# Kernel tuning notes

Measured on AMD Instinct MI355X. Metric: run time of the kernel, lower is better.

## Reference

```python
import jax, jax.numpy as jnp
import numpy as np

FEAT_STRIDE = 16
NEG_THR, POS_THR = 0.3, 0.7        # cfg.TRAIN.RPN_NEGATIVE_OVERLAP / RPN_POSITIVE_OVERLAP
RPN_BATCHSIZE, NUM_FG = 256, 128   # RPN_BATCHSIZE, FG_FRACTION=0.5
A_PER_LOC = 9


def generate_anchors(base_size=16, ratios=(0.5, 1.0, 2.0), scales=(8, 16, 32)):
    w = h = float(base_size)
    xc = yc = 0.5 * (base_size - 1)
    size = w * h
    ws = np.round(np.sqrt(size / np.array(ratios)))
    hs = np.round(ws * np.array(ratios))
    out = []
    for wi, hi in zip(ws, hs):
        for s in scales:
            W, H = wi * s, hi * s
            out.append([xc - 0.5 * (W - 1), yc - 0.5 * (H - 1),
                        xc + 0.5 * (W - 1), yc + 0.5 * (H - 1)])
    return np.array(out, dtype=np.float32)  # [9, 4]


def _forward(rpn_cls_score, gt_boxes, im_info):
    B, _, H, W = rpn_cls_score.shape
    A = A_PER_LOC
    base = jnp.asarray(generate_anchors())
    sx, sy = jnp.meshgrid(jnp.arange(W) * FEAT_STRIDE, jnp.arange(H) * FEAT_STRIDE)  # 'xy', [H,W]
    shifts = jnp.stack([sx.ravel(), sy.ravel(), sx.ravel(), sy.ravel()], 1).astype(jnp.float32)  # [K,4]
    anchors = (base[None, :, :] + shifts[:, None, :]).reshape(-1, 4)  # [N=K*A, 4], (h,w,a)-major
    N = anchors.shape[0]

    img_h, img_w = im_info[0, 0], im_info[0, 1]
    inside = ((anchors[:, 0] >= 0) & (anchors[:, 1] >= 0) &
              (anchors[:, 2] < img_w) & (anchors[:, 3] < img_h))  # [N]

    # ---- IoU overlaps (torch +1 pixel convention) ----
    gt = gt_boxes[..., :4]  # [B,Kg,4]
    aw = anchors[:, 2] - anchors[:, 0] + 1.0
    ah = anchors[:, 3] - anchors[:, 1] + 1.0
    a_area = aw * ah                                   # [N]
    g_area = (gt[..., 2] - gt[..., 0] + 1.0) * (gt[..., 3] - gt[..., 1] + 1.0)  # [B,Kg]
    ix = jnp.maximum(0.0, jnp.minimum(anchors[None, :, None, 2], gt[:, None, :, 2])
                     - jnp.maximum(anchors[None, :, None, 0], gt[:, None, :, 0]) + 1.0)
    iy = jnp.maximum(0.0, jnp.minimum(anchors[None, :, None, 3], gt[:, None, :, 3])
                     - jnp.maximum(anchors[None, :, None, 1], gt[:, None, :, 1]) + 1.0)
    inter = ix * iy
    ovr = inter / (a_area[None, :, None] + g_area[:, None, :] - inter)  # [B,N,Kg]

    max_ovr = ovr.max(2)
    arg = ovr.argmax(2)                                 # [B,N]
    ovr_in = jnp.where(inside[None, :, None], ovr, 0.0)  # only in-image anchors compete for gt-max
    gt_max = ovr_in.max(1)                              # [B,Kg]
    gt_max = jnp.where(gt_max == 0.0, 1e-5, gt_max)
    is_best = (ovr_in == gt_max[:, None, :]).any(2)     # [B,N]

    # ---- label assignment (RPN_CLOBBER_POSITIVES = False) ----
    lbl = jnp.full((B, N), -1.0, jnp.float32)
    lbl = jnp.where(inside[None] & (max_ovr < NEG_THR), 0.0, lbl)
    lbl = jnp.where(inside[None] & is_best, 1.0, lbl)
    lbl = jnp.where(inside[None] & (max_ovr >= POS_THR), 1.0, lbl)

    # ---- random fg/bg subsampling (deterministic jax PRNG replaces np.random.permutation) ----
    def _subsample(lbl_b, key):
        kf, kb = jax.random.split(key)
        def disable(l, mask, limit, k):
            prio = jnp.where(mask, jax.random.uniform(k, l.shape), -1.0)
            order = jnp.argsort(-prio)
            rank = jnp.zeros(l.shape[0], jnp.int32).at[order].set(jnp.arange(l.shape[0], dtype=jnp.int32))
            return jnp.where(mask & (rank >= limit), -1.0, l)
        lbl_b = disable(lbl_b, lbl_b == 1.0, NUM_FG, kf)
        num_bg = RPN_BATCHSIZE - jnp.sum(lbl_b == 1.0)
        return disable(lbl_b, lbl_b == 0.0, num_bg, kb)

    lbl = jax.vmap(_subsample)(lbl, jax.random.split(jax.random.key(42), B))

    assigned = jnp.take_along_axis(gt, arg[..., None], axis=1)  # [B,N,4]
    acx = anchors[:, 0] + 0.5 * (aw - 1.0)
    acy = anchors[:, 1] + 0.5 * (ah - 1.0)
    g_w = assigned[..., 2] - assigned[..., 0] + 1.0
    g_h = assigned[..., 3] - assigned[..., 1] + 1.0
    gcx = assigned[..., 0] + 0.5 * (g_w - 1.0)
    gcy = assigned[..., 1] + 0.5 * (g_h - 1.0)
    targets = jnp.stack([(gcx - acx[None]) / aw[None], (gcy - acy[None]) / ah[None],
                         jnp.log(g_w / aw[None]), jnp.log(g_h / ah[None])], -1)  # [B,N,4]

    in_w = jnp.where(lbl == 1.0, 1.0, 0.0)             # RPN_BBOX_INSIDE_WEIGHTS = 1
    num_examples = jnp.sum(lbl >= 0.0, axis=1).astype(jnp.float32)  # RPN_POSITIVE_WEIGHT = -1
    uw = 1.0 / num_examples                             # uniform pos/neg weight, per batch
    out_w = jnp.where((lbl == 1.0) | (lbl == 0.0), uw[:, None], 0.0)

    # ---- _unmap with fill=0 for out-of-image anchors ----
    lbl = jnp.where(inside[None], lbl, 0.0)
    targets = jnp.where(inside[None, :, None], targets, 0.0)
    in_w = jnp.where(inside[None], in_w, 0.0)
    out_w = jnp.where(inside[None], out_w, 0.0)

    labels_out = lbl.reshape(B, H, W, A).transpose(0, 3, 1, 2).reshape(B, 1, A * H, W)
    targets_out = targets.reshape(B, H, W, 4 * A).transpose(0, 3, 1, 2)
    in_w_out = jnp.broadcast_to(in_w[..., None], (B, N, 4)).reshape(B, H, W, 4 * A).transpose(0, 3, 1, 2)
    out_w_out = jnp.broadcast_to(out_w[..., None], (B, N, 4)).reshape(B, H, W, 4 * A).transpose(0, 3, 1, 2)
    return labels_out, targets_out, in_w_out, out_w_out


def setup_inputs() -> dict:
    key = jax.random.key(0)
    B, A, H, W, Kg = 16, 9, 64, 64, 50
    k1, k2, k3, k4, k5 = jax.random.split(key, 5)
    rpn_cls_score = jax.random.normal(k1, (B, 2 * A, H, W), jnp.float32)
    # valid GT boxes inside a 1024x1024 image, class label in column 4
    x1 = jax.random.uniform(k2, (B, Kg)) * 800.0
    y1 = jax.random.uniform(k3, (B, Kg)) * 800.0
    w = 20.0 + jax.random.uniform(k4, (B, Kg)) * 200.0
    h = 20.0 + jax.random.uniform(k5, (B, Kg)) * 200.0
    cls = jnp.ones((B, Kg), jnp.float32)
    gt_boxes = jnp.stack([x1, y1, x1 + w, y1 + h, cls], -1)
    im_info = jnp.full((B, 2), 1024.0, jnp.float32)
    return {"rpn_cls_score": rpn_cls_score, "gt_boxes": gt_boxes, "im_info": im_info, "num_boxes": Kg}


def reference(rpn_cls_score, gt_boxes, im_info, num_boxes):
    return _forward(rpn_cls_score, gt_boxes, im_info)
```

## Files before the change

### kernel.cpp

```cpp
#include <hip/hip_runtime.h>
#include <stdint.h>


#define B_   16
#define A_   9
#define H_   64
#define W_   64
#define HW_  (H_*W_)
#define N_   (HW_*A_)
#define KG_  50
#define S0_  (B_*A_*HW_)
#define S1_  (B_*4*A_*HW_)
#define NGTB_ (B_*KG_)
#define CAP_  20480
#define NHIST_ (B_*2*256 + B_*2)

typedef unsigned long long ull;

__constant__ float c_base[A_][4] = {
  { -84.f,  -40.f,  99.f,  55.f},
  {-176.f,  -88.f, 191.f, 103.f},
  {-360.f, -184.f, 375.f, 199.f},
  { -56.f,  -56.f,  71.f,  71.f},
  {-120.f, -120.f, 135.f, 135.f},
  {-248.f, -248.f, 263.f, 263.f},
  { -36.f,  -80.f,  51.f,  95.f},
  { -80.f, -168.f,  95.f, 183.f},
  {-168.f, -344.f, 183.f, 359.f},
};

__device__ __forceinline__ void tf2x32(uint32_t k0, uint32_t k1,
                                       uint32_t x0, uint32_t x1,
                                       uint32_t& o0, uint32_t& o1) {
  const uint32_t ks2 = k0 ^ k1 ^ 0x1BD11BDAu;
  uint32_t ks[3] = {k0, k1, ks2};
  x0 += ks[0]; x1 += ks[1];
  const int R[2][4] = {{13,15,26,6},{17,29,16,24}};
  #pragma unroll
  for (int i = 0; i < 5; i++) {
    #pragma unroll
    for (int j = 0; j < 4; j++) {
      x0 += x1;
      int r = R[i & 1][j];
      x1 = (x1 << r) | (x1 >> (32 - r));
      x1 ^= x0;
    }
    x0 += ks[(i + 1) % 3];
    x1 += ks[(i + 2) % 3] + (uint32_t)(i + 1);
  }
  o0 = x0; o1 = x1;
}

__device__ __attribute__((noinline))
float box_area_f(float x1, float y1, float x2, float y2) {
#pragma clang fp contract(off)
  return (x2 - x1 + 1.f) * (y2 - y1 + 1.f);
}

__device__ __attribute__((noinline))
float iou_core(float ax1, float ay1, float ax2, float ay2, float aarea,
               float gx1, float gy1, float gx2, float gy2, float garea) {
#pragma clang fp contract(off)
  float ix = fmaxf(fminf(ax2, gx2) - fmaxf(ax1, gx1) + 1.f, 0.f);
  float iy = fmaxf(fminf(ay2, gy2) - fmaxf(ay1, gy1) + 1.f, 0.f);
  float inter = ix * iy;
  return inter / (aarea + garea - inter);
}

__global__ __launch_bounds__(256) void k_gtmax(const float* __restrict__ gtb,
                                               const float* __restrict__ iminfo,
                                               float* __restrict__ gt_max,
                                               uint32_t* __restrict__ keys,
                                               int* __restrict__ cnt_hist) {
  const int b = blockIdx.x / KG_;
  const int g = blockIdx.x % KG_;
  const int tid = threadIdx.x;
  if (blockIdx.x == 0 && tid < B_) {
    uint32_t k0, k1, kf0, kf1, kb0, kb1;
    tf2x32(0u, 42u, 0u, (uint32_t)tid, k0, k1);
    tf2x32(k0, k1, 0u, 0u, kf0, kf1);
    tf2x32(k0, k1, 0u, 1u, kb0, kb1);
    keys[tid * 4 + 0] = kf0;
    keys[tid * 4 + 1] = kf1;
    keys[tid * 4 + 2] = kb0;
    keys[tid * 4 + 3] = kb1;
  }
  if (blockIdx.x < 32) {
    const int per = (NHIST_ + 31) / 32;
    const int base = blockIdx.x * per;
    const int lim = min(base + per, NHIST_);
    for (int i = base + tid; i < lim; i += 256) cnt_hist[i] = 0;
  }
  const float* gp = gtb + (b * KG_ + g) * 5;
  const float gx1 = gp[0], gy1 = gp[1], gx2 = gp[2], gy2 = gp[3];
  const float garea = box_area_f(gx1, gy1, gx2, gy2);
  const float imh = iminfo[0], imw = iminfo[1];
  float best = 0.f;
  for (int a = 0; a < A_; a++) {
    const float bx1 = c_base[a][0], by1 = c_base[a][1];
    const float bx2 = c_base[a][2], by2 = c_base[a][3];
    const float aarea = box_area_f(bx1, by1, bx2, by2);
    int xlo = max(0, (int)ceilf(-bx1 / 16.f));
    int xhi = min(W_ - 1, (int)ceilf((imw - bx2) / 16.f) - 1);
    int ylo = max(0, (int)ceilf(-by1 / 16.f));
    int yhi = min(H_ - 1, (int)ceilf((imh - by2) / 16.f) - 1);
    xlo = max(xlo, (int)floorf((gx1 - 1.f - bx2) / 16.f));
    xhi = min(xhi, (int)ceilf((gx2 + 1.f - bx1) / 16.f));
    ylo = max(ylo, (int)floorf((gy1 - 1.f - by2) / 16.f));
    yhi = min(yhi, (int)ceilf((gy2 + 1.f - by1) / 16.f));
    const int nx = xhi - xlo + 1, ny = yhi - ylo + 1;
    if (nx <= 0 || ny <= 0) continue;
    const int lw = (nx <= 1) ? 0 : (32 - __clz(nx - 1));
    const int tot = ny << lw;
    const int mask = (1 << lw) - 1;
    for (int t = tid; t < tot; t += 256) {
      const int xi = t & mask;
      if (xi >= nx) continue;
      const int x = xlo + xi;
      const int y = ylo + (t >> lw);
      const float sx = 16.f * (float)x, sy = 16.f * (float)y;
      best = fmaxf(best, iou_core(bx1 + sx, by1 + sy, bx2 + sx, by2 + sy,
                                  aarea, gx1, gy1, gx2, gy2, garea));
    }
  }
  best = fmaxf(best, __shfl_xor(best, 32));
  best = fmaxf(best, __shfl_xor(best, 16));
  best = fmaxf(best, __shfl_xor(best, 8));
  best = fmaxf(best, __shfl_xor(best, 4));
  best = fmaxf(best, __shfl_xor(best, 2));
  best = fmaxf(best, __shfl_xor(best, 1));
  __shared__ float sw[4];
  if ((tid & 63) == 0) sw[tid >> 6] = best;
  __syncthreads();
  if (tid == 0)
    gt_max[b * KG_ + g] = fmaxf(fmaxf(sw[0], sw[1]), fmaxf(sw[2], sw[3]));
}

__global__ __launch_bounds__(256) void k_fuse(const float* __restrict__ gtb,
                                              const float* __restrict__ iminfo,
                                              const float* __restrict__ gt_max,
                                              const uint32_t* __restrict__ keys,
                                              int* __restrict__ packed,
                                              ull* __restrict__ cand,
                                              int* __restrict__ cnt,
                                              int* __restrict__ hist) {
  __shared__ float sgx1[KG_], sgy1[KG_], sgx2[KG_], sgy2[KG_], sga[KG_], sgm[KG_];
  __shared__ int s_xlo[A_], s_ylo[A_], s_nx[A_], s_pre[A_ + 1];
  __shared__ uint32_t s_k[4];
  __shared__ int s_num[2], s_base[2];
  const int b = blockIdx.y;
  const int tid = threadIdx.x;
  if (tid < KG_) {
    const float* g = gtb + (b * KG_ + tid) * 5;
    float x1 = g[0], y1 = g[1], x2 = g[2], y2 = g[3];
    sgx1[tid] = x1; sgy1[tid] = y1; sgx2[tid] = x2; sgy2[tid] = y2;
    sga[tid] = box_area_f(x1, y1, x2, y2);
    float gm = gt_max[b * KG_ + tid];
    sgm[tid] = (gm == 0.f) ? 1e-5f : gm;
  }
  if (tid < 4) s_k[tid] = keys[b * 4 + tid];
  if (tid < A_) {
    const float imh = iminfo[0], imw = iminfo[1];
    const float bx1 = c_base[tid][0], by1 = c_base[tid][1];
    const float bx2 = c_base[tid][2], by2 = c_base[tid][3];
    int xlo = max(0, (int)ceilf(-bx1 / 16.f));
    int xhi = min(W_ - 1, (int)ceilf((imw - bx2) / 16.f) - 1);
    int ylo = max(0, (int)ceilf(-by1 / 16.f));
    int yhi = min(H_ - 1, (int)ceilf((imh - by2) / 16.f) - 1);
    int nx = max(0, xhi - xlo + 1), ny = max(0, yhi - ylo + 1);
    s_xlo[tid] = xlo; s_ylo[tid] = ylo; s_nx[tid] = nx;
    s_pre[tid + 1] = nx * ny;
  }
  __syncthreads();
  if (tid == 0) {
    s_pre[0] = 0;
    for (int a = 0; a < A_; a++) s_pre[a + 1] += s_pre[a];
  }
  __syncthreads();
  const int C = s_pre[A_];
  const int stride = gridDim.x * 256;

  for (int t0 = blockIdx.x * 256; t0 < C; t0 += stride) {
    if (tid < 2) s_num[tid] = 0;
    __syncthreads();
    const int t = t0 + tid;
    bool act = false;
    int p = 0, lpos = 0, n = 0;
    uint32_t m = 0;
    if (t < C) {
      int a = 0;
      while (t >= s_pre[a + 1]) a++;
      const int idx = t - s_pre[a];
      const int nx = s_nx[a];
      const int y = s_ylo[a] + idx / nx;
      const int x = s_xlo[a] + (idx - (idx / nx) * nx);
      n = (y * W_ + x) * A_ + a;
      const int n2 = a * HW_ + y * W_ + x;
      const float sx = 16.f * (float)x, sy = 16.f * (float)y;
      const float ax1 = c_base[a][0] + sx, ay1 = c_base[a][1] + sy;
      const float ax2 = c_base[a][2] + sx, ay2 = c_base[a][3] + sy;
      const float aarea = box_area_f(c_base[a][0], c_base[a][1],
                                     c_base[a][2], c_base[a][3]);
      float mo = -1.f;
      int bidx = 0;
      bool best = false;
      for (int k = 0; k < KG_; k++) {
        float ovr = iou_core(ax1, ay1, ax2, ay2, aarea,
                             sgx1[k], sgy1[k], sgx2[k], sgy2[k], sga[k]);
        if (ovr > mo) { mo = ovr; bidx = k; }
        best = best || (ovr == sgm[k]);
      }
      int lab = -1;
      if (mo < 0.3f) lab = 0;
      if (best || mo >= 0.7f) lab = 1;
      packed[(size_t)b * N_ + n2] = (bidx << 2) | (lab + 1);
      if (lab >= 0) {
        act = true;
        p = (lab == 1) ? 0 : 1;
        uint32_t y0, y1;
        tf2x32(s_k[2 * p], s_k[2 * p + 1], 0u, (uint32_t)n, y0, y1);
        m = (y0 ^ y1) >> 9;
        lpos = atomicAdd(&s_num[p], 1);
      }
    }
    __syncthreads();
    if (tid < 2 && s_num[tid] > 0)
      s_base[tid] = atomicAdd(&cnt[b * 2 + tid], s_num[tid]);
    __syncthreads();
    if (act) {
      cand[(size_t)(b * 2 + p) * CAP_ + s_base[p] + lpos] =
          ((ull)m << 16) | (ull)(65535 - n);
      atomicAdd(&hist[(b * 2 + p) * 256 + (int)(m >> 15)], 1);
    }
    __syncthreads();
  }
}

__global__ __launch_bounds__(256) void k_select(const ull* __restrict__ cand,
                                                const int* __restrict__ cnt,
                                                const int* __restrict__ hist,
                                                ull* __restrict__ Kstar,
                                                float* __restrict__ uw) {
  const int b = blockIdx.x >> 1, p = blockIdx.x & 1;
  const int tid = threadIdx.x;
  __shared__ ull s_keys[2048];
  __shared__ int s_bin, s_r, s_n;
  const int cf = cnt[b * 2 + 0], cb = cnt[b * 2 + 1];
  const int limit = (p == 0) ? 128 : 256 - min(cf, 128);
  const int c = (p == 0) ? cf : cb;
  if (p == 1 && tid == 0) {
    int kf = min(cf, 128);
    int kb = min(cb, 256 - kf);
    uw[b] = 1.f / (float)(kf + kb);
  }
  if (c <= limit) {
    if (tid == 0) Kstar[b * 2 + p] = 0ull;
    return;
  }
  if (tid == 0) {
    const int* Hh = hist + (b * 2 + p) * 256;
    int acc = 0, bin = 255, r = 0;
    for (; bin >= 0; bin--) {
      int hv = Hh[bin];
      if (acc + hv >= limit) { r = limit - acc; break; }
      acc += hv;
    }
    s_bin = bin; s_r = r; s_n = 0;
  }
  __syncthreads();
  const uint32_t bin0 = (uint32_t)s_bin;
  const int r0 = s_r;
  const ull* C = cand + (size_t)(b * 2 + p) * CAP_;
  for (int i = tid; i < c; i += 256) {
    ull k = C[i];
    if ((uint32_t)(k >> 31) == bin0) {
      int pos = atomicAdd(&s_n, 1);
      if (pos < 2048) s_keys[pos] = k;
    }
  }
  __syncthreads();
  const int s = min(s_n, 2048);
  for (int j = tid; j < s; j += 256) {
    ull kj = s_keys[j];
    int rank = 0;
    for (int q = 0; q < s; q++) rank += (s_keys[q] > kj) ? 1 : 0;
    if (rank == r0 - 1) Kstar[b * 2 + p] = kj;
  }
}

__global__ __launch_bounds__(256) void k_out(const float* __restrict__ gtb,
                                             const float* __restrict__ iminfo,
                                             const int* __restrict__ packed,
                                             const ull* __restrict__ Kstar,
                                             const float* __restrict__ uw,
                                             const uint32_t* __restrict__ keys,
                                             float* __restrict__ out) {
  const int gid = blockIdx.x * 256 + threadIdx.x;
  const int e = gid * 4;
  const int w0 = e & 63;
  const int h = (e >> 6) & 63;
  const int a = (e >> 12) % A_;
  const int b = e / (A_ * HW_);

  const float imh = iminfo[0], imw = iminfo[1];
  const float ay1 = c_base[a][1] + 16.f * (float)h;
  const float ay2 = c_base[a][3] + 16.f * (float)h;
  const bool insY = (ay1 >= 0.f) && (ay2 < imh);

  const int4 pk4 = *(const int4*)(packed + e);
  const int pk[4] = {pk4.x, pk4.y, pk4.z, pk4.w};
  const float uwb = uw[b];
  const ull KF_ = Kstar[b * 2 + 0];
  const ull KB_ = Kstar[b * 2 + 1];
  const uint32_t kf0 = keys[b * 4 + 0], kf1 = keys[b * 4 + 1];
  const uint32_t kb0 = keys[b * 4 + 2], kb1 = keys[b * 4 + 3];

  float4 lab4, tx4, ty4, tw4, th4, inw4, oww4;
  float* labp = (float*)&lab4;
  float* txp = (float*)&tx4; float* typ = (float*)&ty4;
  float* twp = (float*)&tw4; float* thp = (float*)&th4;
  float* inwp = (float*)&inw4; float* owwp = (float*)&oww4;

  #pragma unroll
  for (int j = 0; j < 4; j++) {
    const int w = w0 + j;
    const float ax1 = c_base[a][0] + 16.f * (float)w;
    const float ax2 = c_base[a][2] + 16.f * (float)w;
    const bool ins = insY && (ax1 >= 0.f) && (ax2 < imw);
    int lab = (pk[j] & 3) - 1;
    const int g = pk[j] >> 2;
    float tx = 0.f, ty = 0.f, tw = 0.f, th = 0.f;
    if (ins) {
      if (lab >= 0) {
        const int n = (h * W_ + w) * A_ + a;
        const int p = (lab == 1) ? 0 : 1;
        uint32_t y0, y1;
        tf2x32(p ? kb0 : kf0, p ? kb1 : kf1, 0u, (uint32_t)n, y0, y1);
        ull key = ((ull)((y0 ^ y1) >> 9) << 16) | (ull)(65535 - n);
        if (key < (p ? KB_ : KF_)) lab = -1;
      }
      const float* gp = gtb + ((size_t)b * KG_ + g) * 5;
      float aw = ax2 - ax1 + 1.f, ah = ay2 - ay1 + 1.f;
      float acx = ax1 + 0.5f * (aw - 1.f), acy = ay1 + 0.5f * (ah - 1.f);
      float gw = gp[2] - gp[0] + 1.f, gh = gp[3] - gp[1] + 1.f;
      float gcx = gp[0] + 0.5f * (gw - 1.f), gcy = gp[1] + 0.5f * (gh - 1.f);
      tx = (gcx - acx) / aw;
      ty = (gcy - acy) / ah;
      tw = logf(gw / aw);
      th = logf(gh / ah);
    }
    labp[j] = ins ? (float)lab : 0.f;
    txp[j] = tx; typ[j] = ty; twp[j] = tw; thp[j] = th;
    inwp[j] = (ins && lab == 1) ? 1.f : 0.f;
    owwp[j] = (ins && lab >= 0) ? uwb : 0.f;
  }

  *(float4*)(out + e) = lab4;
  float* o1 = out + S0_;
  const size_t toff = (size_t)b * (4 * A_ * HW_) + (4 * a) * HW_ + h * W_ + w0;
  *(float4*)(o1 + toff)           = tx4;
  *(float4*)(o1 + toff + HW_)     = ty4;
  *(float4*)(o1 + toff + 2 * HW_) = tw4;
  *(float4*)(o1 + toff + 3 * HW_) = th4;
  float* o2 = out + S0_ + S1_;
  *(float4*)(o2 + toff)           = inw4;
  *(float4*)(o2 + toff + HW_)     = inw4;
  *(float4*)(o2 + toff + 2 * HW_) = inw4;
  *(float4*)(o2 + toff + 3 * HW_) = inw4;
  float* o3 = out + S0_ + 2 * (size_t)S1_;
  *(float4*)(o3 + toff)           = oww4;
  *(float4*)(o3 + toff + HW_)     = oww4;
  *(float4*)(o3 + toff + 2 * HW_) = oww4;
  *(float4*)(o3 + toff + 3 * HW_) = oww4;
}

extern "C" void kernel_launch(void* const* d_in, const int* in_sizes, int n_in,
                              void* d_out, int out_size, void* d_ws, size_t ws_size,
                              hipStream_t stream) {
  const float* gtb = (const float*)d_in[1];
  const float* iminfo = (const float*)d_in[2];
  float* out = (float*)d_out;

  int* packed = (int*)d_ws;
  float* gt_max = (float*)(packed + (size_t)B_ * N_);
  float* uw = gt_max + B_ * KG_;
  uint32_t* keys = (uint32_t*)(uw + B_);
  int* cnt = (int*)(keys + B_ * 4);
  int* hist = cnt + B_ * 2;
  ull* Kstar = (ull*)(hist + B_ * 2 * 256);
  ull* cand = Kstar + B_ * 2;

  k_gtmax<<<NGTB_, 256, 0, stream>>>(gtb, iminfo, gt_max, keys, cnt);
  k_fuse<<<dim3(73, B_), 256, 0, stream>>>(gtb, iminfo, gt_max, keys,
                                           packed, cand, cnt, hist);
  k_select<<<B_ * 2, 256, 0, stream>>>(cand, cnt, hist, Kstar, uw);
  k_out<<<S0_ / 4 / 256, 256, 0, stream>>>(gtb, iminfo, packed, Kstar, uw,
                                           keys, out);
}
```

Measured before the change: 137.1 us.

## Merge four kernel launches into one cooperative kernel with grid syncs

Replaces the gt-max, fuse, select and output kernels with a single cooperative kernel of 576 blocks. The stages are separated by grid.sync(), each stage uses grid-stride loops over its virtual blocks, and shared memory is shared between stages through a union. The aim is to remove three kernel launch gaps and the drain between kernels. In exchange, a grid-wide barrier is needed between stages, the final stage is limited to exactly GRID_*256*4 elements, and every stage runs with a fixed grid size that may not suit it.

```diff
diff --git a/kernel.cpp b/kernel.cpp
--- a/kernel.cpp
+++ b/kernel.cpp
@@ -1,5 +1,8 @@
 #include <hip/hip_runtime.h>
+#include <hip/hip_cooperative_groups.h>
 #include <stdint.h>
+
+namespace cg = cooperative_groups;
 
 
 #define B_   16
@@ -12,6 +15,8 @@
 #define S0_  (B_*A_*HW_)
 #define S1_  (B_*4*A_*HW_)
 #define NGTB_ (B_*KG_)
+#define NFB_  (B_*73)
+#define GRID_ 576
 #define CAP_  20480
 #define NHIST_ (B_*2*256 + B_*2)
 
@@ -67,15 +72,38 @@
   return inter / (aarea + garea - inter);
 }
 
-__global__ __launch_bounds__(256) void k_gtmax(const float* __restrict__ gtb,
-                                               const float* __restrict__ iminfo,
-                                               float* __restrict__ gt_max,
-                                               uint32_t* __restrict__ keys,
-                                               int* __restrict__ cnt_hist) {
-  const int b = blockIdx.x / KG_;
-  const int g = blockIdx.x % KG_;
+__global__ __launch_bounds__(256) void k_mega(const float* __restrict__ gtb,
+                                              const float* __restrict__ iminfo,
+                                              float* __restrict__ out,
+                                              int* __restrict__ packed,
+                                              float* __restrict__ gt_max,
+                                              float* __restrict__ uw,
+                                              uint32_t* __restrict__ keys,
+                                              int* __restrict__ cnt,
+                                              int* __restrict__ hist,
+                                              ull* __restrict__ Kstar,
+                                              ull* __restrict__ cand) {
+  cg::grid_group grid = cg::this_grid();
   const int tid = threadIdx.x;
-  if (blockIdx.x == 0 && tid < B_) {
+  const int bid = blockIdx.x;
+
+  __shared__ union {
+    struct {
+      float sgx1[KG_], sgy1[KG_], sgx2[KG_], sgy2[KG_], sga[KG_], sgm[KG_];
+      int xlo[A_], ylo[A_], nx[A_], pre[A_ + 1];
+      uint32_t k[4];
+      int num[2], base[2];
+    } f;
+    struct {
+      ull keys2[2048];
+      int bin, r, n;
+    } s;
+    float sw[4];
+  } sh;
+
+  const float imh = iminfo[0], imw = iminfo[1];
+
+  if (bid == 0 && tid < B_) {
     uint32_t k0, k1, kf0, kf1, kb0, kb1;
     tf2x32(0u, 42u, 0u, (uint32_t)tid, k0, k1);
     tf2x32(k0, k1, 0u, 0u, kf0, kf1);
@@ -85,115 +113,106 @@
     keys[tid * 4 + 2] = kb0;
     keys[tid * 4 + 3] = kb1;
   }
-  if (blockIdx.x < 32) {
+  if (bid < 32) {
     const int per = (NHIST_ + 31) / 32;
-    const int base = blockIdx.x * per;
+    const int base = bid * per;
     const int lim = min(base + per, NHIST_);
-    for (int i = base + tid; i < lim; i += 256) cnt_hist[i] = 0;
-  }
-  const float* gp = gtb + (b * KG_ + g) * 5;
-  const float gx1 = gp[0], gy1 = gp[1], gx2 = gp[2], gy2 = gp[3];
-  const float garea = box_area_f(gx1, gy1, gx2, gy2);
-  const float imh = iminfo[0], imw = iminfo[1];
-  float best = 0.f;
-  for (int a = 0; a < A_; a++) {
-    const float bx1 = c_base[a][0], by1 = c_base[a][1];
-    const float bx2 = c_base[a][2], by2 = c_base[a][3];
-    const float aarea = box_area_f(bx1, by1, bx2, by2);
-    int xlo = max(0, (int)ceilf(-bx1 / 16.f));
-    int xhi = min(W_ - 1, (int)ceilf((imw - bx2) / 16.f) - 1);
-    int ylo = max(0, (int)ceilf(-by1 / 16.f));
-    int yhi = min(H_ - 1, (int)ceilf((imh - by2) / 16.f) - 1);
-    xlo = max(xlo, (int)floorf((gx1 - 1.f - bx2) / 16.f));
-    xhi = min(xhi, (int)ceilf((gx2 + 1.f - bx1) / 16.f));
-    ylo = max(ylo, (int)floorf((gy1 - 1.f - by2) / 16.f));
-    yhi = min(yhi, (int)ceilf((gy2 + 1.f - by1) / 16.f));
-    const int nx = xhi - xlo + 1, ny = yhi - ylo + 1;
-    if (nx <= 0 || ny <= 0) continue;
-    const int lw = (nx <= 1) ? 0 : (32 - __clz(nx - 1));
-    const int tot = ny << lw;
-    const int mask = (1 << lw) - 1;
-    for (int t = tid; t < tot; t += 256) {
-      const int xi = t & mask;
-      if (xi >= nx) continue;
-      const int x = xlo + xi;
-      const int y = ylo + (t >> lw);
-      const float sx = 16.f * (float)x, sy = 16.f * (float)y;
-      best = fmaxf(best, iou_core(bx1 + sx, by1 + sy, bx2 + sx, by2 + sy,
-                                  aarea, gx1, gy1, gx2, gy2, garea));
-    }
-  }
-  best = fmaxf(best, __shfl_xor(best, 32));
-  best = fmaxf(best, __shfl_xor(best, 16));
-  best = fmaxf(best, __shfl_xor(best, 8));
-  best = fmaxf(best, __shfl_xor(best, 4));
-  best = fmaxf(best, __shfl_xor(best, 2));
-  best = fmaxf(best, __shfl_xor(best, 1));
-  __shared__ float sw[4];
-  if ((tid & 63) == 0) sw[tid >> 6] = best;
-  __syncthreads();
-  if (tid == 0)
-    gt_max[b * KG_ + g] = fmaxf(fmaxf(sw[0], sw[1]), fmaxf(sw[2], sw[3]));
-}
-
-__global__ __launch_bounds__(256) void k_fuse(const float* __restrict__ gtb,
-                                              const float* __restrict__ iminfo,
-                                              const float* __restrict__ gt_max,
-                                              const uint32_t* __restrict__ keys,
-                                              int* __restrict__ packed,
-                                              ull* __restrict__ cand,
-                                              int* __restrict__ cnt,
-                                              int* __restrict__ hist) {
-  __shared__ float sgx1[KG_], sgy1[KG_], sgx2[KG_], sgy2[KG_], sga[KG_], sgm[KG_];
-  __shared__ int s_xlo[A_], s_ylo[A_], s_nx[A_], s_pre[A_ + 1];
-  __shared__ uint32_t s_k[4];
-  __shared__ int s_num[2], s_base[2];
-  const int b = blockIdx.y;
-  const int tid = threadIdx.x;
-  if (tid < KG_) {
-    const float* g = gtb + (b * KG_ + tid) * 5;
-    float x1 = g[0], y1 = g[1], x2 = g[2], y2 = g[3];
-    sgx1[tid] = x1; sgy1[tid] = y1; sgx2[tid] = x2; sgy2[tid] = y2;
-    sga[tid] = box_area_f(x1, y1, x2, y2);
-    float gm = gt_max[b * KG_ + tid];
-    sgm[tid] = (gm == 0.f) ? 1e-5f : gm;
-  }
-  if (tid < 4) s_k[tid] = keys[b * 4 + tid];
-  if (tid < A_) {
-    const float imh = iminfo[0], imw = iminfo[1];
-    const float bx1 = c_base[tid][0], by1 = c_base[tid][1];
-    const float bx2 = c_base[tid][2], by2 = c_base[tid][3];
-    int xlo = max(0, (int)ceilf(-bx1 / 16.f));
-    int xhi = min(W_ - 1, (int)ceilf((imw - bx2) / 16.f) - 1);
-    int ylo = max(0, (int)ceilf(-by1 / 16.f));
-    int yhi = min(H_ - 1, (int)ceilf((imh - by2) / 16.f) - 1);
-    int nx = max(0, xhi - xlo + 1), ny = max(0, yhi - ylo + 1);
-    s_xlo[tid] = xlo; s_ylo[tid] = ylo; s_nx[tid] = nx;
-    s_pre[tid + 1] = nx * ny;
-  }
-  __syncthreads();
-  if (tid == 0) {
-    s_pre[0] = 0;
-    for (int a = 0; a < A_; a++) s_pre[a + 1] += s_pre[a];
-  }
-  __syncthreads();
-  const int C = s_pre[A_];
-  const int stride = gridDim.x * 256;
-
-  for (int t0 = blockIdx.x * 256; t0 < C; t0 += stride) {
-    if (tid < 2) s_num[tid] = 0;
-    __syncthreads();
-    const int t = t0 + tid;
+    for (int i = base + tid; i < lim; i += 256) cnt[i] = 0;
+  }
+  for (int vb = bid; vb < NGTB_; vb += GRID_) {
+    const int b = vb / KG_;
+    const int g = vb % KG_;
+    const float* gp = gtb + (b * KG_ + g) * 5;
+    const float gx1 = gp[0], gy1 = gp[1], gx2 = gp[2], gy2 = gp[3];
+    const float garea = box_area_f(gx1, gy1, gx2, gy2);
+    float best = 0.f;
+    for (int a = 0; a < A_; a++) {
+      const float bx1 = c_base[a][0], by1 = c_base[a][1];
+      const float bx2 = c_base[a][2], by2 = c_base[a][3];
+      const float aarea = box_area_f(bx1, by1, bx2, by2);
+      int xlo = max(0, (int)ceilf(-bx1 / 16.f));
+      int xhi = min(W_ - 1, (int)ceilf((imw - bx2) / 16.f) - 1);
+      int ylo = max(0, (int)ceilf(-by1 / 16.f));
+      int yhi = min(H_ - 1, (int)ceilf((imh - by2) / 16.f) - 1);
+      xlo = max(xlo, (int)floorf((gx1 - 1.f - bx2) / 16.f));
+      xhi = min(xhi, (int)ceilf((gx2 + 1.f - bx1) / 16.f));
+      ylo = max(ylo, (int)floorf((gy1 - 1.f - by2) / 16.f));
+      yhi = min(yhi, (int)ceilf((gy2 + 1.f - by1) / 16.f));
+      const int nx = xhi - xlo + 1, ny = yhi - ylo + 1;
+      if (nx <= 0 || ny <= 0) continue;
+      const int lw = (nx <= 1) ? 0 : (32 - __clz(nx - 1));
+      const int tot = ny << lw;
+      const int mask = (1 << lw) - 1;
+      for (int t = tid; t < tot; t += 256) {
+        const int xi = t & mask;
+        if (xi >= nx) continue;
+        const int x = xlo + xi;
+        const int y = ylo + (t >> lw);
+        const float sx = 16.f * (float)x, sy = 16.f * (float)y;
+        best = fmaxf(best, iou_core(bx1 + sx, by1 + sy, bx2 + sx, by2 + sy,
+                                    aarea, gx1, gy1, gx2, gy2, garea));
+      }
+    }
+    best = fmaxf(best, __shfl_xor(best, 32));
+    best = fmaxf(best, __shfl_xor(best, 16));
+    best = fmaxf(best, __shfl_xor(best, 8));
+    best = fmaxf(best, __shfl_xor(best, 4));
+    best = fmaxf(best, __shfl_xor(best, 2));
+    best = fmaxf(best, __shfl_xor(best, 1));
+    if ((tid & 63) == 0) sh.sw[tid >> 6] = best;
+    __syncthreads();
+    if (tid == 0)
+      gt_max[b * KG_ + g] = fmaxf(fmaxf(sh.sw[0], sh.sw[1]),
+                                  fmaxf(sh.sw[2], sh.sw[3]));
+    __syncthreads();
+  }
+
+  grid.sync();
+
+  for (int vb = bid; vb < NFB_; vb += GRID_) {
+    const int b = vb / 73;
+    const int chunk = vb % 73;
+    __syncthreads();
+    if (tid < KG_) {
+      const float* g = gtb + (b * KG_ + tid) * 5;
+      float x1 = g[0], y1 = g[1], x2 = g[2], y2 = g[3];
+      sh.f.sgx1[tid] = x1; sh.f.sgy1[tid] = y1;
+      sh.f.sgx2[tid] = x2; sh.f.sgy2[tid] = y2;
+      sh.f.sga[tid] = box_area_f(x1, y1, x2, y2);
+      float gm = gt_max[b * KG_ + tid];
+      sh.f.sgm[tid] = (gm == 0.f) ? 1e-5f : gm;
+    }
+    if (tid < 4) sh.f.k[tid] = keys[b * 4 + tid];
+    if (tid < 2) sh.f.num[tid] = 0;
+    if (tid < A_) {
+      const float bx1 = c_base[tid][0], by1 = c_base[tid][1];
+      const float bx2 = c_base[tid][2], by2 = c_base[tid][3];
+      int xlo = max(0, (int)ceilf(-bx1 / 16.f));
+      int xhi = min(W_ - 1, (int)ceilf((imw - bx2) / 16.f) - 1);
+      int ylo = max(0, (int)ceilf(-by1 / 16.f));
+      int yhi = min(H_ - 1, (int)ceilf((imh - by2) / 16.f) - 1);
+      int nx = max(0, xhi - xlo + 1), ny = max(0, yhi - ylo + 1);
+      sh.f.xlo[tid] = xlo; sh.f.ylo[tid] = ylo; sh.f.nx[tid] = nx;
+      sh.f.pre[tid + 1] = nx * ny;
+    }
+    __syncthreads();
+    if (tid == 0) {
+      sh.f.pre[0] = 0;
+      for (int a = 0; a < A_; a++) sh.f.pre[a + 1] += sh.f.pre[a];
+    }
+    __syncthreads();
+    const int C = sh.f.pre[A_];
+    const int t = chunk * 256 + tid;
     bool act = false;
     int p = 0, lpos = 0, n = 0;
     uint32_t m = 0;
     if (t < C) {
       int a = 0;
-      while (t >= s_pre[a + 1]) a++;
-      const int idx = t - s_pre[a];
-      const int nx = s_nx[a];
-      const int y = s_ylo[a] + idx / nx;
-      const int x = s_xlo[a] + (idx - (idx / nx) * nx);
+      while (t >= sh.f.pre[a + 1]) a++;
+      const int idx = t - sh.f.pre[a];
+      const int nx = sh.f.nx[a];
+      const int y = sh.f.ylo[a] + idx / nx;
+      const int x = sh.f.xlo[a] + (idx - (idx / nx) * nx);
       n = (y * W_ + x) * A_ + a;
       const int n2 = a * HW_ + y * W_ + x;
       const float sx = 16.f * (float)x, sy = 16.f * (float)y;
@@ -206,9 +225,10 @@
       bool best = false;
       for (int k = 0; k < KG_; k++) {
         float ovr = iou_core(ax1, ay1, ax2, ay2, aarea,
-                             sgx1[k], sgy1[k], sgx2[k], sgy2[k], sga[k]);
+                             sh.f.sgx1[k], sh.f.sgy1[k],
+                             sh.f.sgx2[k], sh.f.sgy2[k], sh.f.sga[k]);
         if (ovr > mo) { mo = ovr; bidx = k; }
-        best = best || (ovr == sgm[k]);
+        best = best || (ovr == sh.f.sgm[k]);
       }
       int lab = -1;
       if (mo < 0.3f) lab = 0;
@@ -218,160 +238,149 @@
         act = true;
         p = (lab == 1) ? 0 : 1;
         uint32_t y0, y1;
-        tf2x32(s_k[2 * p], s_k[2 * p + 1], 0u, (uint32_t)n, y0, y1);
+        tf2x32(sh.f.k[2 * p], sh.f.k[2 * p + 1], 0u, (uint32_t)n, y0, y1);
         m = (y0 ^ y1) >> 9;
-        lpos = atomicAdd(&s_num[p], 1);
-      }
-    }
-    __syncthreads();
-    if (tid < 2 && s_num[tid] > 0)
-      s_base[tid] = atomicAdd(&cnt[b * 2 + tid], s_num[tid]);
+        lpos = atomicAdd(&sh.f.num[p], 1);
+      }
+    }
+    __syncthreads();
+    if (tid < 2 && sh.f.num[tid] > 0)
+      sh.f.base[tid] = atomicAdd(&cnt[b * 2 + tid], sh.f.num[tid]);
     __syncthreads();
     if (act) {
-      cand[(size_t)(b * 2 + p) * CAP_ + s_base[p] + lpos] =
+      cand[(size_t)(b * 2 + p) * CAP_ + sh.f.base[p] + lpos] =
           ((ull)m << 16) | (ull)(65535 - n);
       atomicAdd(&hist[(b * 2 + p) * 256 + (int)(m >> 15)], 1);
     }
-    __syncthreads();
-  }
-}
-
-__global__ __launch_bounds__(256) void k_select(const ull* __restrict__ cand,
-                                                const int* __restrict__ cnt,
-                                                const int* __restrict__ hist,
-                                                ull* __restrict__ Kstar,
-                                                float* __restrict__ uw) {
-  const int b = blockIdx.x >> 1, p = blockIdx.x & 1;
-  const int tid = threadIdx.x;
-  __shared__ ull s_keys[2048];
-  __shared__ int s_bin, s_r, s_n;
-  const int cf = cnt[b * 2 + 0], cb = cnt[b * 2 + 1];
-  const int limit = (p == 0) ? 128 : 256 - min(cf, 128);
-  const int c = (p == 0) ? cf : cb;
-  if (p == 1 && tid == 0) {
-    int kf = min(cf, 128);
-    int kb = min(cb, 256 - kf);
-    uw[b] = 1.f / (float)(kf + kb);
-  }
-  if (c <= limit) {
-    if (tid == 0) Kstar[b * 2 + p] = 0ull;
-    return;
-  }
-  if (tid == 0) {
-    const int* Hh = hist + (b * 2 + p) * 256;
-    int acc = 0, bin = 255, r = 0;
-    for (; bin >= 0; bin--) {
-      int hv = Hh[bin];
-      if (acc + hv >= limit) { r = limit - acc; break; }
-      acc += hv;
-    }
-    s_bin = bin; s_r = r; s_n = 0;
-  }
-  __syncthreads();
-  const uint32_t bin0 = (uint32_t)s_bin;
-  const int r0 = s_r;
-  const ull* C = cand + (size_t)(b * 2 + p) * CAP_;
-  for (int i = tid; i < c; i += 256) {
-    ull k = C[i];
-    if ((uint32_t)(k >> 31) == bin0) {
-      int pos = atomicAdd(&s_n, 1);
-      if (pos < 2048) s_keys[pos] = k;
-    }
-  }
-  __syncthreads();
-  const int s = min(s_n, 2048);
-  for (int j = tid; j < s; j += 256) {
-    ull kj = s_keys[j];
-    int rank = 0;
-    for (int q = 0; q < s; q++) rank += (s_keys[q] > kj) ? 1 : 0;
-    if (rank == r0 - 1) Kstar[b * 2 + p] = kj;
-  }
-}
-
-__global__ __launch_bounds__(256) void k_out(const float* __restrict__ gtb,
-                                             const float* __restrict__ iminfo,
-                                             const int* __restrict__ packed,
-                                             const ull* __restrict__ Kstar,
-                                             const float* __restrict__ uw,
-                                             const uint32_t* __restrict__ keys,
-                                             float* __restrict__ out) {
-  const int gid = blockIdx.x * 256 + threadIdx.x;
-  const int e = gid * 4;
-  const int w0 = e & 63;
-  const int h = (e >> 6) & 63;
-  const int a = (e >> 12) % A_;
-  const int b = e / (A_ * HW_);
-
-  const float imh = iminfo[0], imw = iminfo[1];
-  const float ay1 = c_base[a][1] + 16.f * (float)h;
-  const float ay2 = c_base[a][3] + 16.f * (float)h;
-  const bool insY = (ay1 >= 0.f) && (ay2 < imh);
-
-  const int4 pk4 = *(const int4*)(packed + e);
-  const int pk[4] = {pk4.x, pk4.y, pk4.z, pk4.w};
-  const float uwb = uw[b];
-  const ull KF_ = Kstar[b * 2 + 0];
-  const ull KB_ = Kstar[b * 2 + 1];
-  const uint32_t kf0 = keys[b * 4 + 0], kf1 = keys[b * 4 + 1];
-  const uint32_t kb0 = keys[b * 4 + 2], kb1 = keys[b * 4 + 3];
-
-  float4 lab4, tx4, ty4, tw4, th4, inw4, oww4;
-  float* labp = (float*)&lab4;
-  float* txp = (float*)&tx4; float* typ = (float*)&ty4;
-  float* twp = (float*)&tw4; float* thp = (float*)&th4;
-  float* inwp = (float*)&inw4; float* owwp = (float*)&oww4;
-
-  #pragma unroll
-  for (int j = 0; j < 4; j++) {
-    const int w = w0 + j;
-    const float ax1 = c_base[a][0] + 16.f * (float)w;
-    const float ax2 = c_base[a][2] + 16.f * (float)w;
-    const bool ins = insY && (ax1 >= 0.f) && (ax2 < imw);
-    int lab = (pk[j] & 3) - 1;
-    const int g = pk[j] >> 2;
-    float tx = 0.f, ty = 0.f, tw = 0.f, th = 0.f;
-    if (ins) {
-      if (lab >= 0) {
-        const int n = (h * W_ + w) * A_ + a;
-        const int p = (lab == 1) ? 0 : 1;
-        uint32_t y0, y1;
-        tf2x32(p ? kb0 : kf0, p ? kb1 : kf1, 0u, (uint32_t)n, y0, y1);
-        ull key = ((ull)((y0 ^ y1) >> 9) << 16) | (ull)(65535 - n);
-        if (key < (p ? KB_ : KF_)) lab = -1;
-      }
-      const float* gp = gtb + ((size_t)b * KG_ + g) * 5;
-      float aw = ax2 - ax1 + 1.f, ah = ay2 - ay1 + 1.f;
-      float acx = ax1 + 0.5f * (aw - 1.f), acy = ay1 + 0.5f * (ah - 1.f);
-      float gw = gp[2] - gp[0] + 1.f, gh = gp[3] - gp[1] + 1.f;
-      float gcx = gp[0] + 0.5f * (gw - 1.f), gcy = gp[1] + 0.5f * (gh - 1.f);
-      tx = (gcx - acx) / aw;
-      ty = (gcy - acy) / ah;
-      tw = logf(gw / aw);
-      th = logf(gh / ah);
-    }
-    labp[j] = ins ? (float)lab : 0.f;
-    txp[j] = tx; typ[j] = ty; twp[j] = tw; thp[j] = th;
-    inwp[j] = (ins && lab == 1) ? 1.f : 0.f;
-    owwp[j] = (ins && lab >= 0) ? uwb : 0.f;
-  }
-
-  *(float4*)(out + e) = lab4;
-  float* o1 = out + S0_;
-  const size_t toff = (size_t)b * (4 * A_ * HW_) + (4 * a) * HW_ + h * W_ + w0;
-  *(float4*)(o1 + toff)           = tx4;
-  *(float4*)(o1 + toff + HW_)     = ty4;
-  *(float4*)(o1 + toff + 2 * HW_) = tw4;
-  *(float4*)(o1 + toff + 3 * HW_) = th4;
-  float* o2 = out + S0_ + S1_;
-  *(float4*)(o2 + toff)           = inw4;
-  *(float4*)(o2 + toff + HW_)     = inw4;
-  *(float4*)(o2 + toff + 2 * HW_) = inw4;
-  *(float4*)(o2 + toff + 3 * HW_) = inw4;
-  float* o3 = out + S0_ + 2 * (size_t)S1_;
-  *(float4*)(o3 + toff)           = oww4;
-  *(float4*)(o3 + toff + HW_)     = oww4;
-  *(float4*)(o3 + toff + 2 * HW_) = oww4;
-  *(float4*)(o3 + toff + 3 * HW_) = oww4;
+  }
+
+  grid.sync();
+
+  if (bid < B_ * 2) {
+    const int b = bid >> 1, p = bid & 1;
+    const int cf = cnt[b * 2 + 0], cb = cnt[b * 2 + 1];
+    const int limit = (p == 0) ? 128 : 256 - min(cf, 128);
+    const int c = (p == 0) ? cf : cb;
+    if (p == 1 && tid == 0) {
+      int kf = min(cf, 128);
+      int kb = min(cb, 256 - kf);
+      uw[b] = 1.f / (float)(kf + kb);
+    }
+    if (c <= limit) {
+      if (tid == 0) Kstar[b * 2 + p] = 0ull;
+    } else {
+      if (tid == 0) {
+        const int* Hh = hist + (b * 2 + p) * 256;
+        int acc = 0, bin = 255, r = 0;
+        for (; bin >= 0; bin--) {
+          int hv = Hh[bin];
+          if (acc + hv >= limit) { r = limit - acc; break; }
+          acc += hv;
+        }
+        sh.s.bin = bin; sh.s.r = r; sh.s.n = 0;
+      }
+      __syncthreads();
+      const uint32_t bin0 = (uint32_t)sh.s.bin;
+      const int r0 = sh.s.r;
+      const ull* C = cand + (size_t)(b * 2 + p) * CAP_;
+      for (int i = tid; i < c; i += 256) {
+        ull k = C[i];
+        if ((uint32_t)(k >> 31) == bin0) {
+          int pos = atomicAdd(&sh.s.n, 1);
+          if (pos < 2048) sh.s.keys2[pos] = k;
+        }
+      }
+      __syncthreads();
+      const int s = min(sh.s.n, 2048);
+      for (int j = tid; j < s; j += 256) {
+        ull kj = sh.s.keys2[j];
+        int rank = 0;
+        for (int q = 0; q < s; q++) rank += (sh.s.keys2[q] > kj) ? 1 : 0;
+        if (rank == r0 - 1) Kstar[b * 2 + p] = kj;
+      }
+    }
+  }
+
+  grid.sync();
+
+  {
+    const int gid = bid * 256 + tid;
+    const int e = gid * 4;
+    const int w0 = e & 63;
+    const int h = (e >> 6) & 63;
+    const int a = (e >> 12) % A_;
+    const int b = e / (A_ * HW_);
+
+    const float ay1 = c_base[a][1] + 16.f * (float)h;
+    const float ay2 = c_base[a][3] + 16.f * (float)h;
+    const bool insY = (ay1 >= 0.f) && (ay2 < imh);
+
+    const int4 pk4 = *(const int4*)(packed + e);
+    const int pk[4] = {pk4.x, pk4.y, pk4.z, pk4.w};
+    const float uwb = uw[b];
+    const ull KF_ = Kstar[b * 2 + 0];
+    const ull KB_ = Kstar[b * 2 + 1];
+    const uint32_t kf0 = keys[b * 4 + 0], kf1 = keys[b * 4 + 1];
+    const uint32_t kb0 = keys[b * 4 + 2], kb1 = keys[b * 4 + 3];
+
+    float4 lab4, tx4, ty4, tw4, th4, inw4, oww4;
+    float* labp = (float*)&lab4;
+    float* txp = (float*)&tx4; float* typ = (float*)&ty4;
+    float* twp = (float*)&tw4; float* thp = (float*)&th4;
+    float* inwp = (float*)&inw4; float* owwp = (float*)&oww4;
+
+    #pragma unroll
+    for (int j = 0; j < 4; j++) {
+      const int w = w0 + j;
+      const float ax1 = c_base[a][0] + 16.f * (float)w;
+      const float ax2 = c_base[a][2] + 16.f * (float)w;
+      const bool ins = insY && (ax1 >= 0.f) && (ax2 < imw);
+      int lab = (pk[j] & 3) - 1;
+      const int g = pk[j] >> 2;
+      float tx = 0.f, ty = 0.f, tw = 0.f, th = 0.f;
+      if (ins) {
+        if (lab >= 0) {
+          const int n = (h * W_ + w) * A_ + a;
+          const int p = (lab == 1) ? 0 : 1;
+          uint32_t y0, y1;
+          tf2x32(p ? kb0 : kf0, p ? kb1 : kf1, 0u, (uint32_t)n, y0, y1);
+          ull key = ((ull)((y0 ^ y1) >> 9) << 16) | (ull)(65535 - n);
+          if (key < (p ? KB_ : KF_)) lab = -1;
+        }
+        const float* gp = gtb + ((size_t)b * KG_ + g) * 5;
+        float aw = ax2 - ax1 + 1.f, ah = ay2 - ay1 + 1.f;
+        float acx = ax1 + 0.5f * (aw - 1.f), acy = ay1 + 0.5f * (ah - 1.f);
+        float gw = gp[2] - gp[0] + 1.f, gh = gp[3] - gp[1] + 1.f;
+        float gcx = gp[0] + 0.5f * (gw - 1.f), gcy = gp[1] + 0.5f * (gh - 1.f);
+        tx = (gcx - acx) / aw;
+        ty = (gcy - acy) / ah;
+        tw = logf(gw / aw);
+        th = logf(gh / ah);
+      }
+      labp[j] = ins ? (float)lab : 0.f;
+      txp[j] = tx; typ[j] = ty; twp[j] = tw; thp[j] = th;
+      inwp[j] = (ins && lab == 1) ? 1.f : 0.f;
+      owwp[j] = (ins && lab >= 0) ? uwb : 0.f;
+    }
+
+    *(float4*)(out + e) = lab4;
+    float* o1 = out + S0_;
+    const size_t toff = (size_t)b * (4 * A_ * HW_) + (4 * a) * HW_ + h * W_ + w0;
+    *(float4*)(o1 + toff)           = tx4;
+    *(float4*)(o1 + toff + HW_)     = ty4;
+    *(float4*)(o1 + toff + 2 * HW_) = tw4;
+    *(float4*)(o1 + toff + 3 * HW_) = th4;
+    float* o2 = out + S0_ + S1_;
+    *(float4*)(o2 + toff)           = inw4;
+    *(float4*)(o2 + toff + HW_)     = inw4;
+    *(float4*)(o2 + toff + 2 * HW_) = inw4;
+    *(float4*)(o2 + toff + 3 * HW_) = inw4;
+    float* o3 = out + S0_ + 2 * (size_t)S1_;
+    *(float4*)(o3 + toff)           = oww4;
+    *(float4*)(o3 + toff + HW_)     = oww4;
+    *(float4*)(o3 + toff + 2 * HW_) = oww4;
+    *(float4*)(o3 + toff + 3 * HW_) = oww4;
+  }
 }
 
 extern "C" void kernel_launch(void* const* d_in, const int* in_sizes, int n_in,
@@ -390,10 +399,11 @@
   ull* Kstar = (ull*)(hist + B_ * 2 * 256);
   ull* cand = Kstar + B_ * 2;
 
-  k_gtmax<<<NGTB_, 256, 0, stream>>>(gtb, iminfo, gt_max, keys, cnt);
-  k_fuse<<<dim3(73, B_), 256, 0, stream>>>(gtb, iminfo, gt_max, keys,
-                                           packed, cand, cnt, hist);
-  k_select<<<B_ * 2, 256, 0, stream>>>(cand, cnt, hist, Kstar, uw);
-  k_out<<<S0_ / 4 / 256, 256, 0, stream>>>(gtb, iminfo, packed, Kstar, uw,
-                                           keys, out);
+  void* args[] = {
+    (void*)&gtb, (void*)&iminfo, (void*)&out, (void*)&packed,
+    (void*)&gt_max, (void*)&uw, (void*)&keys, (void*)&cnt,
+    (void*)&hist, (void*)&Kstar, (void*)&cand,
+  };
+  hipLaunchCooperativeKernel((const void*)k_mega, dim3(GRID_), dim3(256),
+                             args, 0, stream);
 }
```

After: 341.9 us. 2.49x slower.

## Fuse top-k selection into fuse kernel via last-block-done counter

Applied to the files above, without the earlier changes.

Removes the separate selection kernel. The last k_fuse block to finish for each batch, detected with an atomic done counter and thread fences, performs the histogram-bin threshold search and rank selection for both foreground and background. This saves a kernel launch and its inter-kernel gap. In exchange, the selection for the two classes runs serially in one block per batch, and every k_fuse block now reserves 16 KB of extra shared memory, which may lower occupancy.

```diff
diff --git a/kernel.cpp b/kernel.cpp
--- a/kernel.cpp
+++ b/kernel.cpp
@@ -12,8 +12,9 @@
 #define S0_  (B_*A_*HW_)
 #define S1_  (B_*4*A_*HW_)
 #define NGTB_ (B_*KG_)
+#define FB_   73
 #define CAP_  20480
-#define NHIST_ (B_*2*256 + B_*2)
+#define NCLR_ (B_*2*256 + B_*2 + B_)
 
 typedef unsigned long long ull;
 
@@ -86,9 +87,9 @@
     keys[tid * 4 + 3] = kb1;
   }
   if (blockIdx.x < 32) {
-    const int per = (NHIST_ + 31) / 32;
+    const int per = (NCLR_ + 31) / 32;
     const int base = blockIdx.x * per;
-    const int lim = min(base + per, NHIST_);
+    const int lim = min(base + per, NCLR_);
     for (int i = base + tid; i < lim; i += 256) cnt_hist[i] = 0;
   }
   const float* gp = gtb + (b * KG_ + g) * 5;
@@ -143,11 +144,16 @@
                                               int* __restrict__ packed,
                                               ull* __restrict__ cand,
                                               int* __restrict__ cnt,
-                                              int* __restrict__ hist) {
+                                              int* __restrict__ hist,
+                                              int* __restrict__ done,
+                                              ull* __restrict__ Kstar,
+                                              float* __restrict__ uw) {
   __shared__ float sgx1[KG_], sgy1[KG_], sgx2[KG_], sgy2[KG_], sga[KG_], sgm[KG_];
   __shared__ int s_xlo[A_], s_ylo[A_], s_nx[A_], s_pre[A_ + 1];
   __shared__ uint32_t s_k[4];
   __shared__ int s_num[2], s_base[2];
+  __shared__ ull s_keys[2048];
+  __shared__ int s_bin, s_r, s_n, s_last;
   const int b = blockIdx.y;
   const int tid = threadIdx.x;
   if (tid < KG_) {
@@ -234,57 +240,56 @@
     }
     __syncthreads();
   }
-}
-
-__global__ __launch_bounds__(256) void k_select(const ull* __restrict__ cand,
-                                                const int* __restrict__ cnt,
-                                                const int* __restrict__ hist,
-                                                ull* __restrict__ Kstar,
-                                                float* __restrict__ uw) {
-  const int b = blockIdx.x >> 1, p = blockIdx.x & 1;
-  const int tid = threadIdx.x;
-  __shared__ ull s_keys[2048];
-  __shared__ int s_bin, s_r, s_n;
+
+  __threadfence();
+  if (tid == 0) s_last = (atomicAdd(&done[b], 1) == FB_ - 1);
+  __syncthreads();
+  if (!s_last) return;
+  __threadfence();
+
   const int cf = cnt[b * 2 + 0], cb = cnt[b * 2 + 1];
-  const int limit = (p == 0) ? 128 : 256 - min(cf, 128);
-  const int c = (p == 0) ? cf : cb;
-  if (p == 1 && tid == 0) {
+  {
     int kf = min(cf, 128);
     int kb = min(cb, 256 - kf);
-    uw[b] = 1.f / (float)(kf + kb);
-  }
-  if (c <= limit) {
-    if (tid == 0) Kstar[b * 2 + p] = 0ull;
-    return;
-  }
-  if (tid == 0) {
-    const int* Hh = hist + (b * 2 + p) * 256;
-    int acc = 0, bin = 255, r = 0;
-    for (; bin >= 0; bin--) {
-      int hv = Hh[bin];
-      if (acc + hv >= limit) { r = limit - acc; break; }
-      acc += hv;
-    }
-    s_bin = bin; s_r = r; s_n = 0;
-  }
-  __syncthreads();
-  const uint32_t bin0 = (uint32_t)s_bin;
-  const int r0 = s_r;
-  const ull* C = cand + (size_t)(b * 2 + p) * CAP_;
-  for (int i = tid; i < c; i += 256) {
-    ull k = C[i];
-    if ((uint32_t)(k >> 31) == bin0) {
-      int pos = atomicAdd(&s_n, 1);
-      if (pos < 2048) s_keys[pos] = k;
-    }
-  }
-  __syncthreads();
-  const int s = min(s_n, 2048);
-  for (int j = tid; j < s; j += 256) {
-    ull kj = s_keys[j];
-    int rank = 0;
-    for (int q = 0; q < s; q++) rank += (s_keys[q] > kj) ? 1 : 0;
-    if (rank == r0 - 1) Kstar[b * 2 + p] = kj;
+    if (tid == 0) uw[b] = 1.f / (float)(kf + kb);
+  }
+  for (int p = 0; p < 2; p++) {
+    const int limit = (p == 0) ? 128 : 256 - min(cf, 128);
+    const int c = (p == 0) ? cf : cb;
+    if (c <= limit) {
+      if (tid == 0) Kstar[b * 2 + p] = 0ull;
+      continue;
+    }
+    if (tid == 0) {
+      const int* Hh = hist + (b * 2 + p) * 256;
+      int acc = 0, bin = 255, r = 0;
+      for (; bin >= 0; bin--) {
+        int hv = Hh[bin];
+        if (acc + hv >= limit) { r = limit - acc; break; }
+        acc += hv;
+      }
+      s_bin = bin; s_r = r; s_n = 0;
+    }
+    __syncthreads();
+    const uint32_t bin0 = (uint32_t)s_bin;
+    const int r0 = s_r;
+    const ull* Cc = cand + (size_t)(b * 2 + p) * CAP_;
+    for (int i = tid; i < c; i += 256) {
+      ull k = Cc[i];
+      if ((uint32_t)(k >> 31) == bin0) {
+        int pos = atomicAdd(&s_n, 1);
+        if (pos < 2048) s_keys[pos] = k;
+      }
+    }
+    __syncthreads();
+    const int s = min(s_n, 2048);
+    for (int j = tid; j < s; j += 256) {
+      ull kj = s_keys[j];
+      int rank = 0;
+      for (int q = 0; q < s; q++) rank += (s_keys[q] > kj) ? 1 : 0;
+      if (rank == r0 - 1) Kstar[b * 2 + p] = kj;
+    }
+    __syncthreads();
   }
 }
 
@@ -387,13 +392,14 @@
   uint32_t* keys = (uint32_t*)(uw + B_);
   int* cnt = (int*)(keys + B_ * 4);
   int* hist = cnt + B_ * 2;
-  ull* Kstar = (ull*)(hist + B_ * 2 * 256);
+  int* done = hist + B_ * 2 * 256;
+  ull* Kstar = (ull*)(done + B_);
   ull* cand = Kstar + B_ * 2;
 
   k_gtmax<<<NGTB_, 256, 0, stream>>>(gtb, iminfo, gt_max, keys, cnt);
-  k_fuse<<<dim3(73, B_), 256, 0, stream>>>(gtb, iminfo, gt_max, keys,
-                                           packed, cand, cnt, hist);
-  k_select<<<B_ * 2, 256, 0, stream>>>(cand, cnt, hist, Kstar, uw);
+  k_fuse<<<dim3(FB_, B_), 256, 0, stream>>>(gtb, iminfo, gt_max, keys,
+                                            packed, cand, cnt, hist,
+                                            done, Kstar, uw);
   k_out<<<S0_ / 4 / 256, 256, 0, stream>>>(gtb, iminfo, packed, Kstar, uw,
                                            keys, out);
 }
```

Result: slower. 233.4 us (+70.3%).
